# Optimization experiments

Hardware: AMD Instinct MI355X
Metric: run time of the kernel (lower is better)

Reference implementation:

```python
import jax, jax.numpy as jnp
import numpy as np

D = 1024      # d_model
E = 8         # initial_experts
H = 4 * D     # expert FFN hidden
CAP_F = 1.25  # capacity_factor
VOCAB = 256


def setup_inputs() -> dict:
    key = jax.random.key(0)
    ks = jax.random.split(key, 10)
    w = lambda k, shape, s: jax.random.normal(k, shape, jnp.float32) * s
    return dict(
        byte_seq=jax.random.randint(ks[0], (4, 2048), 0, VOCAB, jnp.int32),
        emb=w(ks[1], (VOCAB, D), 0.02),
        Wp=w(ks[2], (D, D), 1.0 / np.sqrt(D)), bp=jnp.zeros((D,), jnp.float32),
        Wg=w(ks[3], (D, D), 1.0 / np.sqrt(D)), bg=jnp.zeros((D,), jnp.float32),
        Wr=w(ks[4], (D, E), 1.0 / np.sqrt(D)), br=jnp.zeros((E,), jnp.float32),
        W1=w(ks[5], (E, D, H), 1.0 / np.sqrt(D)), b1=jnp.zeros((E, H), jnp.float32),
        W2=w(ks[6], (E, H, D), 1.0 / np.sqrt(H)), b2=jnp.zeros((E, D), jnp.float32),
        Wh=w(ks[7], (D, VOCAB), 1.0 / np.sqrt(D)), bh=jnp.zeros((VOCAB,), jnp.float32),
    )


def reference(byte_seq, emb, Wp, bp, Wg, bg, Wr, br, W1, b1, W2, b2, Wh, bh):
    # ---- byte embedding ----
    x = emb[byte_seq]                                 # [B,T,D]
    B, T, _ = x.shape

    # ---- SSM core: precompute input projections, scan only the recurrence ----
    px = x @ Wp + bp                                   # [B,T,D]
    gx = jax.nn.sigmoid(x @ Wg + bg)                   # [B,T,D]

    def step(state, inp):
        p, g = inp
        state = jnp.tanh(p + state)
        return state, g * state

    s0 = jnp.zeros((B, D), x.dtype)
    next_state, ys = jax.lax.scan(step, s0, (px.transpose(1, 0, 2), gx.transpose(1, 0, 2)))
    y = ys.transpose(1, 0, 2)                          # [B,T,D]

    # ---- capacity-limited top-1 MoE routing ----
    xf = y.reshape(-1, D)                              # [N,D]
    N = xf.shape[0]
    probs = jax.nn.softmax(xf @ Wr + br, axis=-1)      # [N,E]
    top = jnp.argmax(probs, axis=-1)                   # [N]
    onehot = jax.nn.one_hot(top, E, dtype=xf.dtype)    # [N,E]
    pos = jnp.cumsum(onehot, axis=0) * onehot          # 1-based slot within expert
    capacity = int(CAP_F * N / E)
    keep = (pos > 0) & (pos <= capacity)               # [N,E] tokens within capacity
    gate = jnp.take_along_axis(probs, top[:, None], axis=-1)[:, 0]  # [N]
    scale = gate * keep.any(axis=-1).astype(xf.dtype)

    # grouped expert FFN (fixed small loop over experts, masked combine)
    out = jnp.zeros_like(xf)
    for e in range(E):
        h = jax.nn.gelu(xf @ W1[e] + b1[e])            # [N,H]
        oe = h @ W2[e] + b2[e]                         # [N,D]
        out = out + oe * keep[:, e].astype(xf.dtype)[:, None]
    out = out * scale[:, None]

    entropy_loss = -jnp.mean(jnp.sum(probs * jnp.log(probs + 1e-9), axis=-1))
    expert_counts = jnp.sum(onehot, axis=0)

    logits = out.reshape(B, T, D) @ Wh + bh            # [B,T,256]
    return logits, next_state, entropy_loss, expert_counts
```

## Files before the change

### kernel.cpp

```cpp
#include <hip/hip_runtime.h>
#include <hip/hip_bf16.h>
#include <cstdint>
#include <cstddef>

#define AS1 __attribute__((address_space(1)))
#define AS3 __attribute__((address_space(3)))

typedef __hip_bfloat16 bf16;
typedef float f32x4 __attribute__((ext_vector_type(4)));
typedef short bf16x8 __attribute__((ext_vector_type(8)));

#define B_     4
#define T_     2048
#define D_     1024
#define E_     8
#define H_     4096
#define NTOK   8192
#define CAP    1280
#define VOCAB_ 256

static constexpr size_t OFF_PG    = 0;
static constexpr size_t OFF_Y     = 2097152;
static constexpr size_t OFF_TOP   = 35651584;
static constexpr size_t OFF_GATE  = 35684352;
static constexpr size_t OFF_ENT   = 35717120;
static constexpr size_t OFF_CNT   = 35749888;
static constexpr size_t OFF_CKEPT = 35750144;
static constexpr size_t OFF_SLOT  = 35750400;
static constexpr size_t OFF_XE    = 35791360;
static constexpr size_t OFF_HE    = 56762880;
static constexpr size_t OFF_WT    = 140648960;
static constexpr size_t OFF_WHT   = 207757824;
static constexpr size_t OFF_OUTB  = 208282112;

#define LOGITS_OFF 0
#define NS_OFF     2097152
#define ENT_OFF    2101248
#define CNT_OFF    2101249

__device__ __forceinline__ void gll16(const void* g, void* l) {
  __builtin_amdgcn_global_load_lds((AS1 const void*)g, (AS3 void*)l, 16, 0, 0);
}
__device__ __forceinline__ unsigned short f2bu(float f) {
  bf16 h = __float2bfloat16(f);
  return __builtin_bit_cast(unsigned short, h);
}
__device__ __forceinline__ float bu2f(unsigned short u) {
  unsigned int x = ((unsigned int)u) << 16;
  return __builtin_bit_cast(float, x);
}
__device__ __forceinline__ float fast_tanh(float z) {
  float e2 = __expf(z + z);
  return fmaf(-2.f, __builtin_amdgcn_rcpf(e2 + 1.f), 1.f);
}

__global__ __launch_bounds__(256) void slv_embproj_part(
    const float* __restrict__ emb, const float* __restrict__ Wp,
    const float* __restrict__ Wg,
    float* __restrict__ Ppart, float* __restrict__ Gpart) {
  __shared__ float embT[128][9];
  int rb = blockIdx.x, kc = blockIdx.y;
  int r0 = rb * 8, k0 = kc * 128;
  int tid = threadIdx.x;
  int c = tid * 4;
  {
    int i4 = tid * 4;
    int r = i4 >> 7, kb = i4 & 127;
    f32x4 v = *reinterpret_cast<const f32x4*>(emb + (size_t)(r0 + r) * D_ + k0 + kb);
    embT[kb + 0][r] = v.x; embT[kb + 1][r] = v.y;
    embT[kb + 2][r] = v.z; embT[kb + 3][r] = v.w;
  }
  __syncthreads();
  f32x4 aP[8] = {}, aG[8] = {};
  #pragma unroll 4
  for (int kk = 0; kk < 128; ++kk) {
    f32x4 wp = *reinterpret_cast<const f32x4*>(Wp + (size_t)(k0 + kk) * D_ + c);
    f32x4 wg = *reinterpret_cast<const f32x4*>(Wg + (size_t)(k0 + kk) * D_ + c);
    #pragma unroll
    for (int r = 0; r < 8; ++r) {
      float e = embT[kk][r];
      aP[r] += e * wp;
      aG[r] += e * wg;
    }
  }
  #pragma unroll
  for (int r = 0; r < 8; ++r) {
    size_t o = ((size_t)kc * 256 + r0 + r) * D_ + c;
    *reinterpret_cast<f32x4*>(Ppart + o) = aP[r];
    *reinterpret_cast<f32x4*>(Gpart + o) = aG[r];
  }
}

__global__ __launch_bounds__(256) void slv_embproj_reduce(
    const float* __restrict__ Ppart, const float* __restrict__ Gpart,
    const float* __restrict__ bp, const float* __restrict__ bg,
    float2* __restrict__ PG) {
  int i = blockIdx.x * 256 + threadIdx.x;
  int r = i >> 8;
  int c = (i & 255) * 4;
  f32x4 sp = {}, sg = {};
  #pragma unroll
  for (int kc = 0; kc < 8; ++kc) {
    size_t o = ((size_t)kc * 256 + r) * D_ + c;
    sp += *reinterpret_cast<const f32x4*>(Ppart + o);
    sg += *reinterpret_cast<const f32x4*>(Gpart + o);
  }
  sp += *reinterpret_cast<const f32x4*>(bp + c);
  sg += *reinterpret_cast<const f32x4*>(bg + c);
  f32x4 g;
  g.x = 1.f / (1.f + __expf(-sg.x));
  g.y = 1.f / (1.f + __expf(-sg.y));
  g.z = 1.f / (1.f + __expf(-sg.z));
  g.w = 1.f / (1.f + __expf(-sg.w));
  f32x4 st0 = { sp.x, g.x, sp.y, g.y };
  f32x4 st1 = { sp.z, g.z, sp.w, g.w };
  f32x4* dst = reinterpret_cast<f32x4*>(PG + (size_t)r * D_ + c);
  dst[0] = st0; dst[1] = st1;
}

__global__ __launch_bounds__(256) void slv_gatherpg(
    const int* __restrict__ bytes, const float2* __restrict__ PG,
    float2* __restrict__ pg_seq) {
  int t0 = blockIdx.x * 16;
  __shared__ int bl[16];
  if (threadIdx.x < 16) bl[threadIdx.x] = bytes[t0 + threadIdx.x];
  __syncthreads();
  int c = threadIdx.x * 4;
  #pragma unroll 4
  for (int u = 0; u < 16; ++u) {
    const f32x4* src = (const f32x4*)(PG + (size_t)bl[u] * D_ + c);
    f32x4* dst = (f32x4*)(pg_seq + (size_t)(t0 + u) * D_ + c);
    f32x4 v0 = src[0], v1 = src[1];
    dst[0] = v0; dst[1] = v1;
  }
}

#define SU 16
__global__ __launch_bounds__(64, 1) void slv_scan(
    const float2* __restrict__ pg_seq,
    float* __restrict__ y, float* __restrict__ ns) {
  int b = blockIdx.x >> 4;
  int d = (blockIdx.x & 15) * 64 + threadIdx.x;
  const float2* pp = pg_seq + (size_t)b * T_ * D_ + d;
  float* yp = y + (size_t)b * T_ * D_ + d;
  float2 pA[SU], pB[SU];
  #pragma unroll
  for (int u = 0; u < SU; ++u) pA[u] = pp[(size_t)u * D_];
  float s = 0.f;
  for (int t0 = 0; t0 < T_; t0 += 2 * SU) {
    #pragma unroll
    for (int u = 0; u < SU; ++u) pB[u] = pp[(size_t)(t0 + SU + u) * D_];
    #pragma unroll
    for (int u = 0; u < SU; ++u) {
      s = fast_tanh(pA[u].x + s);
      yp[(size_t)(t0 + u) * D_] = pA[u].y * s;
    }
    if (t0 + 2 * SU < T_) {
      #pragma unroll
      for (int u = 0; u < SU; ++u) pA[u] = pp[(size_t)(t0 + 2 * SU + u) * D_];
    }
    #pragma unroll
    for (int u = 0; u < SU; ++u) {
      s = fast_tanh(pB[u].x + s);
      yp[(size_t)(t0 + SU + u) * D_] = pB[u].y * s;
    }
  }
  ns[b * D_ + d] = s;
}

__global__ __launch_bounds__(256) void slv_router(
    const float* __restrict__ y, const float* __restrict__ Wr, const float* __restrict__ br,
    int* __restrict__ top, float* __restrict__ gate, float* __restrict__ entTok,
    int* __restrict__ countsInt) {
  int wave = threadIdx.x >> 6, lane = threadIdx.x & 63;
  int tok = blockIdx.x * 4 + wave;
  const float* yr = y + (size_t)tok * D_;
  float acc[E_];
  #pragma unroll
  for (int e = 0; e < E_; ++e) acc[e] = 0.f;
  for (int i = 0; i < 16; ++i) {
    int d = i * 64 + lane;
    float v = yr[d];
    const float4* w = (const float4*)(Wr + d * E_);
    float4 w0 = w[0], w1 = w[1];
    acc[0] = fmaf(v, w0.x, acc[0]); acc[1] = fmaf(v, w0.y, acc[1]);
    acc[2] = fmaf(v, w0.z, acc[2]); acc[3] = fmaf(v, w0.w, acc[3]);
    acc[4] = fmaf(v, w1.x, acc[4]); acc[5] = fmaf(v, w1.y, acc[5]);
    acc[6] = fmaf(v, w1.z, acc[6]); acc[7] = fmaf(v, w1.w, acc[7]);
  }
  #pragma unroll
  for (int off = 32; off; off >>= 1)
    #pragma unroll
    for (int e = 0; e < E_; ++e) acc[e] += __shfl_xor(acc[e], off);
  if (lane == 0) {
    float l[E_], p[E_];
    float mx = -1e30f;
    #pragma unroll
    for (int e = 0; e < E_; ++e) { l[e] = acc[e] + br[e]; mx = fmaxf(mx, l[e]); }
    float sum = 0.f;
    #pragma unroll
    for (int e = 0; e < E_; ++e) { p[e] = expf(l[e] - mx); sum += p[e]; }
    float inv = 1.f / sum;
    int bestE = 0; float bestP = -1.f; float ent = 0.f;
    #pragma unroll
    for (int e = 0; e < E_; ++e) {
      float pe = p[e] * inv;
      ent += pe * logf(pe + 1e-9f);
      if (pe > bestP) { bestP = pe; bestE = e; }
    }
    top[tok] = bestE; gate[tok] = bestP; entTok[tok] = ent;
    atomicAdd(&countsInt[bestE], 1);
  }
}

__global__ __launch_bounds__(256) void slv_capacity(
    const int* __restrict__ top, int* __restrict__ slotTok, int* __restrict__ cntKept) {
  __shared__ unsigned char tops[NTOK];
  __shared__ int sb[256];
  int tid = threadIdx.x;
  for (int i = tid; i < NTOK; i += 256) tops[i] = (unsigned char)top[i];
  __syncthreads();
  int cnt[E_];
  #pragma unroll
  for (int e = 0; e < E_; ++e) cnt[e] = 0;
  int n0 = tid * 32;
  for (int i = 0; i < 32; ++i) {
    int v = tops[n0 + i];
    #pragma unroll
    for (int e = 0; e < E_; ++e) cnt[e] += (v == e) ? 1 : 0;
  }
  int base[E_];
  for (int e = 0; e < E_; ++e) {
    sb[tid] = cnt[e];
    __syncthreads();
    for (int off = 1; off < 256; off <<= 1) {
      int add = (tid >= off) ? sb[tid - off] : 0;
      __syncthreads();
      sb[tid] += add;
      __syncthreads();
    }
    base[e] = sb[tid] - cnt[e];
    if (tid == 0) cntKept[e] = min(sb[255], CAP);
    __syncthreads();
  }
  for (int i = 0; i < 32; ++i) {
    int n = n0 + i;
    int v = tops[n];
    #pragma unroll
    for (int e = 0; e < E_; ++e) {
      if (v == e) {
        int r = base[e]++;
        if (r < CAP) slotTok[e * CAP + r] = n;
      }
    }
  }
}

__global__ __launch_bounds__(256) void slv_gather(
    const float* __restrict__ y, const int* __restrict__ slotTok,
    const int* __restrict__ cntKept, unsigned short* __restrict__ Xe) {
  int slot = blockIdx.x;
  int e = slot / CAP, r = slot % CAP;
  int c4 = threadIdx.x * 4;
  ushort4 o;
  if (r < cntKept[e]) {
    int tok = slotTok[slot];
    float4 v = *(const float4*)(y + (size_t)tok * D_ + c4);
    o.x = f2bu(v.x); o.y = f2bu(v.y); o.z = f2bu(v.z); o.w = f2bu(v.w);
  } else {
    o.x = 0; o.y = 0; o.z = 0; o.w = 0;
  }
  *(ushort4*)(Xe + (size_t)slot * D_ + c4) = o;
}

__global__ __launch_bounds__(256) void slv_transpose(
    const float* __restrict__ in, bf16* __restrict__ out, int R, int C) {
  __shared__ float tile[64][65];
  size_t mat = (size_t)blockIdx.z * R * C;
  int c0 = blockIdx.x * 64, r0 = blockIdx.y * 64;
  int tid = threadIdx.x;
  #pragma unroll
  for (int j = 0; j < 16; ++j) {
    int idx = j * 256 + tid; int r = idx >> 6, c = idx & 63;
    tile[r][c] = in[mat + (size_t)(r0 + r) * C + c0 + c];
  }
  __syncthreads();
  #pragma unroll
  for (int j = 0; j < 4; ++j) {
    int lin = j * 256 + tid;
    int cc = lin >> 4;
    int rr = (lin & 15) * 4;
    ushort4 v;
    v.x = f2bu(tile[rr + 0][cc]); v.y = f2bu(tile[rr + 1][cc]);
    v.z = f2bu(tile[rr + 2][cc]); v.w = f2bu(tile[rr + 3][cc]);
    *(ushort4*)((unsigned short*)out + mat + (size_t)(c0 + cc) * R + r0 + rr) = v;
  }
}

__device__ __forceinline__ void gemm_core(
    const char* ga, const char* gb, int K, bf16* As, bf16* Bs,
    f32x4 (&acc)[4][4], int wave, int lane, int wr, int wc) {
  const int Krow = K * 2;
  for (int ks = 0; ks < K; ks += 64) {
    #pragma unroll
    for (int rnd = 0; rnd < 4; ++rnd) {
      int chunk = rnd * 4 + wave;
      int o = chunk * 1024 + lane * 16;
      int row = o >> 7, col = o & 127;
      int scol = col ^ ((row & 7) << 4);
      size_t gofs = (size_t)row * Krow + (size_t)ks * 2 + scol;
      gll16(ga + gofs, (char*)As + chunk * 1024);
      gll16(gb + gofs, (char*)Bs + chunk * 1024);
    }
    __syncthreads();
    #pragma unroll
    for (int kk = 0; kk < 2; ++kk) {
      bf16x8 a[4], b[4];
      int koff = kk * 64 + ((lane >> 4) << 4);
      #pragma unroll
      for (int m = 0; m < 4; ++m) {
        int row = wr * 64 + m * 16 + (lane & 15);
        int sc = koff ^ ((row & 7) << 4);
        a[m] = *(const bf16x8*)((const char*)As + row * 128 + sc);
      }
      #pragma unroll
      for (int n = 0; n < 4; ++n) {
        int row = wc * 64 + n * 16 + (lane & 15);
        int sc = koff ^ ((row & 7) << 4);
        b[n] = *(const bf16x8*)((const char*)Bs + row * 128 + sc);
      }
      #pragma unroll
      for (int m = 0; m < 4; ++m)
        #pragma unroll
        for (int n = 0; n < 4; ++n)
          acc[m][n] = __builtin_amdgcn_mfma_f32_16x16x32_bf16(a[m], b[n], acc[m][n], 0, 0, 0);
    }
    __syncthreads();
  }
}

__device__ __forceinline__ void gemm256_core(
    const char* ga, const char* gb, size_t krow, size_t kbyte0, int NT,
    char* lds, int tid, int lane, int wr, int wc, f32x4 (&acc)[8][4]) {
  auto STAGE = [&](int kt) {
    char* lb = lds + (kt & 1) * 65536;
    #pragma unroll
    for (int h = 0; h < 4; ++h) {
      const char* g = (h < 2) ? ga : gb;
      #pragma unroll
      for (int c2 = 0; c2 < 2; ++c2) {
        int o = c2 * 8192 + tid * 16;
        int row = o >> 7, col = o & 127;
        int scol = col ^ ((row & 7) << 4);
        size_t gofs = (size_t)((h & 1) * 128 + row) * krow + kbyte0 + (size_t)kt * 128 + scol;
        gll16(g + gofs, lb + h * 16384 + o);
      }
    }
  };
  int koff16 = (lane >> 4) << 4;
  STAGE(0);
  for (int kt = 0; kt < NT; ++kt) {
    __builtin_amdgcn_s_barrier();
    if (kt + 1 < NT) {
      STAGE(kt + 1);
      asm volatile("s_waitcnt vmcnt(8)" ::: "memory");
    } else {
      asm volatile("s_waitcnt vmcnt(0)" ::: "memory");
    }
    __builtin_amdgcn_s_barrier();
    __builtin_amdgcn_sched_barrier(0);
    const char* Ab = lds + (kt & 1) * 65536;
    const char* Bb = Ab + 32768;
    bf16x8 b0[4], b1[4];
    #pragma unroll
    for (int n = 0; n < 4; ++n) {
      int row = wc * 64 + n * 16 + (lane & 15);
      const char* base = Bb + row * 128;
      int sw = (row & 7) << 4;
      b0[n] = *(const bf16x8*)(base + (koff16 ^ sw));
      b1[n] = *(const bf16x8*)(base + ((64 + koff16) ^ sw));
    }
    #pragma unroll
    for (int mp = 0; mp < 4; ++mp) {
      bf16x8 a0[2], a1[2];
      #pragma unroll
      for (int i = 0; i < 2; ++i) {
        int row = wr * 128 + (mp * 2 + i) * 16 + (lane & 15);
        const char* base = Ab + row * 128;
        int sw = (row & 7) << 4;
        a0[i] = *(const bf16x8*)(base + (koff16 ^ sw));
        a1[i] = *(const bf16x8*)(base + ((64 + koff16) ^ sw));
      }
      __builtin_amdgcn_s_setprio(1);
      #pragma unroll
      for (int i = 0; i < 2; ++i) {
        int m = mp * 2 + i;
        #pragma unroll
        for (int n = 0; n < 4; ++n)
          acc[m][n] = __builtin_amdgcn_mfma_f32_16x16x32_bf16(a0[i], b0[n], acc[m][n], 0, 0, 0);
        #pragma unroll
        for (int n = 0; n < 4; ++n)
          acc[m][n] = __builtin_amdgcn_mfma_f32_16x16x32_bf16(a1[i], b1[n], acc[m][n], 0, 0, 0);
      }
      __builtin_amdgcn_s_setprio(0);
    }
  }
}

__global__ __launch_bounds__(512, 2) void slv_ffn1_g(
    const bf16* __restrict__ Xe, const bf16* __restrict__ W1t, const float* __restrict__ b1,
    const int* __restrict__ cntKept, unsigned short* __restrict__ He) {
  int e = blockIdx.z, mt = blockIdx.y, nt = blockIdx.x;
  if (mt * 256 >= cntKept[e]) return;
  extern __shared__ char lds[];
  int tid = threadIdx.x, wave = tid >> 6, lane = tid & 63;
  int wr = wave >> 2, wc = wave & 3;
  const char* ga = (const char*)(Xe + ((size_t)e * CAP + mt * 256) * D_);
  const char* gb = (const char*)(W1t + ((size_t)e * H_ + nt * 256) * D_);
  f32x4 acc[8][4] = {};
  gemm256_core(ga, gb, (size_t)D_ * 2, 0, D_ / 64, lds, tid, lane, wr, wc, acc);
  size_t slot0 = (size_t)e * CAP + mt * 256;
  int colb = nt * 256 + wc * 64;
  #pragma unroll
  for (int m = 0; m < 8; ++m) {
    int trow0 = wr * 128 + m * 16 + ((lane >> 4) << 2);
    #pragma unroll
    for (int n = 0; n < 4; ++n) {
      int col = colb + n * 16 + (lane & 15);
      float bias = b1[e * H_ + col];
      #pragma unroll
      for (int r = 0; r < 4; ++r) {
        float x = acc[m][n][r] + bias;
        float t = fast_tanh(0.7978845608028654f * (x + 0.044715f * x * x * x));
        float gel = 0.5f * x * (1.f + t);
        He[(slot0 + trow0 + r) * (size_t)H_ + col] = f2bu(gel);
      }
    }
  }
}

__global__ __launch_bounds__(512, 2) void slv_ffn2_part(
    const bf16* __restrict__ He, const bf16* __restrict__ W2t,
    const int* __restrict__ cntKept,
    unsigned short* __restrict__ part0, unsigned short* __restrict__ part1) {
  int ez = blockIdx.z;
  int e = ez >> 1, s = ez & 1;
  int mt = blockIdx.y, nt = blockIdx.x;
  if (mt * 256 >= cntKept[e]) return;
  extern __shared__ char lds[];
  int tid = threadIdx.x, wave = tid >> 6, lane = tid & 63;
  int wr = wave >> 2, wc = wave & 3;
  const char* ga = (const char*)(He + ((size_t)e * CAP + mt * 256) * H_);
  const char* gb = (const char*)(W2t + ((size_t)e * D_ + nt * 256) * H_);
  f32x4 acc[8][4] = {};
  gemm256_core(ga, gb, (size_t)H_ * 2, (size_t)s * 2048 * 2, 2048 / 64,
               lds, tid, lane, wr, wc, acc);
  unsigned short* part = s ? part1 : part0;
  size_t slot0 = (size_t)e * CAP + mt * 256;
  int colb = nt * 256 + wc * 64;
  #pragma unroll
  for (int m = 0; m < 8; ++m) {
    int trow0 = wr * 128 + m * 16 + ((lane >> 4) << 2);
    #pragma unroll
    for (int n = 0; n < 4; ++n) {
      int col = colb + n * 16 + (lane & 15);
      #pragma unroll
      for (int r = 0; r < 4; ++r)
        part[(slot0 + trow0 + r) * (size_t)D_ + col] = f2bu(acc[m][n][r]);
    }
  }
}

__global__ __launch_bounds__(256) void slv_ffn2_reduce(
    const unsigned short* __restrict__ part0, const unsigned short* __restrict__ part1,
    const float* __restrict__ b2, const int* __restrict__ cntKept,
    const int* __restrict__ slotTok, const float* __restrict__ gate,
    unsigned short* __restrict__ outb) {
  int slot = blockIdx.x;
  int e = slot / CAP, r = slot % CAP;
  if (r >= cntKept[e]) return;
  int tok = slotTok[slot];
  float sc = gate[tok];
  int c4 = threadIdx.x * 4;
  ushort4 p0 = *(const ushort4*)(part0 + (size_t)slot * D_ + c4);
  ushort4 p1 = *(const ushort4*)(part1 + (size_t)slot * D_ + c4);
  const float4 bb = *(const float4*)(b2 + e * D_ + c4);
  ushort4 o;
  o.x = f2bu((bu2f(p0.x) + bu2f(p1.x) + bb.x) * sc);
  o.y = f2bu((bu2f(p0.y) + bu2f(p1.y) + bb.y) * sc);
  o.z = f2bu((bu2f(p0.z) + bu2f(p1.z) + bb.z) * sc);
  o.w = f2bu((bu2f(p0.w) + bu2f(p1.w) + bb.w) * sc);
  *(ushort4*)(outb + (size_t)tok * D_ + c4) = o;
}

__global__ __launch_bounds__(256) void slv_head(
    const bf16* __restrict__ outb, const bf16* __restrict__ Wht, const float* __restrict__ bh,
    float* __restrict__ logits) {
  int nt = blockIdx.x, mt = blockIdx.y;
  __shared__ __align__(16) bf16 As[128 * 64], Bs[128 * 64];
  int tid = threadIdx.x, wave = tid >> 6, lane = tid & 63;
  int wr = wave >> 1, wc = wave & 1;
  const char* ga = (const char*)(outb + (size_t)mt * 128 * D_);
  const char* gb = (const char*)(Wht + (size_t)nt * 128 * D_);
  f32x4 acc[4][4] = {};
  gemm_core(ga, gb, D_, As, Bs, acc, wave, lane, wr, wc);
  int colb = nt * 128 + wc * 64;
  #pragma unroll
  for (int m = 0; m < 4; ++m) {
    int trow0 = wr * 64 + m * 16 + ((lane >> 4) << 2);
    #pragma unroll
    for (int n = 0; n < 4; ++n) {
      int col = colb + n * 16 + (lane & 15);
      float bias = bh[col];
      #pragma unroll
      for (int r = 0; r < 4; ++r) {
        int row = mt * 128 + trow0 + r;
        logits[(size_t)row * VOCAB_ + col] = acc[m][n][r] + bias;
      }
    }
  }
}

__global__ __launch_bounds__(256) void slv_finalize(
    const float* __restrict__ entTok, const int* __restrict__ countsInt,
    float* __restrict__ out) {
  __shared__ float red[256];
  int tid = threadIdx.x;
  float s = 0.f;
  for (int i = tid; i < NTOK; i += 256) s += entTok[i];
  red[tid] = s;
  __syncthreads();
  for (int off = 128; off; off >>= 1) {
    if (tid < off) red[tid] += red[tid + off];
    __syncthreads();
  }
  if (tid == 0) out[ENT_OFF] = -red[0] / (float)NTOK;
  if (tid < E_) out[CNT_OFF + tid] = (float)countsInt[tid];
}

extern "C" void kernel_launch(void* const* d_in, const int* in_sizes, int n_in,
                              void* d_out, int out_size, void* d_ws, size_t ws_size,
                              hipStream_t stream) {
  (void)in_sizes; (void)n_in; (void)out_size; (void)ws_size;
  const int*   byte_seq = (const int*)d_in[0];
  const float* emb = (const float*)d_in[1];
  const float* Wp  = (const float*)d_in[2];
  const float* bp  = (const float*)d_in[3];
  const float* Wg  = (const float*)d_in[4];
  const float* bg  = (const float*)d_in[5];
  const float* Wr  = (const float*)d_in[6];
  const float* br  = (const float*)d_in[7];
  const float* W1  = (const float*)d_in[8];
  const float* b1  = (const float*)d_in[9];
  const float* W2  = (const float*)d_in[10];
  const float* b2  = (const float*)d_in[11];
  const float* Wh  = (const float*)d_in[12];
  const float* bh  = (const float*)d_in[13];
  float* out = (float*)d_out;

  char* ws = (char*)d_ws;
  float2* PG      = (float2*)(ws + OFF_PG);
  float* y        = (float*)(ws + OFF_Y);
  int*   top      = (int*)(ws + OFF_TOP);
  float* gate     = (float*)(ws + OFF_GATE);
  float* entTok   = (float*)(ws + OFF_ENT);
  int*   countsInt= (int*)(ws + OFF_CNT);
  int*   cntKept  = (int*)(ws + OFF_CKEPT);
  int*   slotTok  = (int*)(ws + OFF_SLOT);
  unsigned short* Xe  = (unsigned short*)(ws + OFF_XE);
  unsigned short* He  = (unsigned short*)(ws + OFF_HE);
  bf16*  Wt       = (bf16*)(ws + OFF_WT);
  bf16*  Wht      = (bf16*)(ws + OFF_WHT);
  unsigned short* outb = (unsigned short*)(ws + OFF_OUTB);
  float*  Ppart   = (float*)(ws + OFF_HE);
  float*  Gpart   = (float*)(ws + OFF_HE + 8388608);
  float2* pg_seq  = (float2*)(ws + OFF_HE);
  unsigned short* part0 = (unsigned short*)(ws + OFF_Y);
  unsigned short* part1 = (unsigned short*)(ws + OFF_XE);

  hipFuncSetAttribute(reinterpret_cast<const void*>(slv_ffn1_g),
                      hipFuncAttributeMaxDynamicSharedMemorySize, 131072);
  hipFuncSetAttribute(reinterpret_cast<const void*>(slv_ffn2_part),
                      hipFuncAttributeMaxDynamicSharedMemorySize, 131072);

  hipMemsetAsync(countsInt, 0, E_ * sizeof(int), stream);
  hipMemsetAsync(outb, 0, (size_t)NTOK * D_ * 2, stream);

  slv_embproj_part<<<dim3(32, 8), 256, 0, stream>>>(emb, Wp, Wg, Ppart, Gpart);
  slv_embproj_reduce<<<256, 256, 0, stream>>>(Ppart, Gpart, bp, bg, PG);
  slv_gatherpg<<<NTOK / 16, 256, 0, stream>>>(byte_seq, PG, pg_seq);
  slv_scan<<<64, 64, 0, stream>>>(pg_seq, y, out + NS_OFF);
  slv_router<<<NTOK / 4, 256, 0, stream>>>(y, Wr, br, top, gate, entTok, countsInt);
  slv_capacity<<<1, 256, 0, stream>>>(top, slotTok, cntKept);
  slv_gather<<<E_ * CAP, 256, 0, stream>>>(y, slotTok, cntKept, Xe);

  slv_transpose<<<dim3(4, 16, 1), 256, 0, stream>>>(Wh, Wht, 1024, 256);
  slv_transpose<<<dim3(64, 16, 8), 256, 0, stream>>>(W1, Wt, 1024, 4096);
  slv_ffn1_g<<<dim3(16, 5, 8), 512, 131072, stream>>>((const bf16*)Xe, Wt, b1, cntKept, He);
  slv_transpose<<<dim3(16, 64, 8), 256, 0, stream>>>(W2, Wt, 4096, 1024);
  slv_ffn2_part<<<dim3(4, 5, 16), 512, 131072, stream>>>((const bf16*)He, Wt, cntKept, part0, part1);
  slv_ffn2_reduce<<<E_ * CAP, 256, 0, stream>>>(part0, part1, b2, cntKept, slotTok, gate, outb);
  slv_head<<<dim3(2, 64), 256, 0, stream>>>((const bf16*)outb, Wht, bh, out + LOGITS_OFF);
  slv_finalize<<<1, 256, 0, stream>>>(entTok, countsInt, out);
}
```

Before: 577.5 us.

## Rework expert GEMM core into 4-stage pipeline and use wave-shuffle capacity scan

The shared 256x256 GEMM core used by both expert FFN kernels moves from a double-buffered K=64 loop to a four-slot ring of K=32 stages. Loads are issued three stages ahead and split into two halves interleaved with two MFMA phases, with finer vmcnt waits and barriers, to hide global-load latency. The capacity kernel's 8 serial block-wide LDS prefix scans are replaced by packed 16-bit counters scanned with wavefront shuffles plus a small cross-wave fixup, removing many syncthreads. This adds more barriers per K step and a new LDS row/column remapping whose correctness relies on matching the fragment layout.

```diff
diff --git a/kernel.cpp b/kernel.cpp
--- a/kernel.cpp
+++ b/kernel.cpp
@@ -216,32 +216,49 @@
 __global__ __launch_bounds__(256) void slv_capacity(
     const int* __restrict__ top, int* __restrict__ slotTok, int* __restrict__ cntKept) {
   __shared__ unsigned char tops[NTOK];
-  __shared__ int sb[256];
-  int tid = threadIdx.x;
+  __shared__ unsigned int wt[4][4];
+  int tid = threadIdx.x, lane = tid & 63, w = tid >> 6;
   for (int i = tid; i < NTOK; i += 256) tops[i] = (unsigned char)top[i];
   __syncthreads();
-  int cnt[E_];
-  #pragma unroll
-  for (int e = 0; e < E_; ++e) cnt[e] = 0;
+  unsigned int c0 = 0, c1 = 0, c2 = 0, c3 = 0;
   int n0 = tid * 32;
   for (int i = 0; i < 32; ++i) {
     int v = tops[n0 + i];
-    #pragma unroll
-    for (int e = 0; e < E_; ++e) cnt[e] += (v == e) ? 1 : 0;
-  }
+    unsigned inc = 1u << ((v & 1) << 4);
+    int hi = v >> 1;
+    if (hi == 0) c0 += inc;
+    else if (hi == 1) c1 += inc;
+    else if (hi == 2) c2 += inc;
+    else c3 += inc;
+  }
+  unsigned int s0 = c0, s1 = c1, s2 = c2, s3 = c3;
+  #pragma unroll
+  for (int off = 1; off < 64; off <<= 1) {
+    unsigned int t0 = (unsigned)__shfl_up((int)s0, off);
+    unsigned int t1 = (unsigned)__shfl_up((int)s1, off);
+    unsigned int t2 = (unsigned)__shfl_up((int)s2, off);
+    unsigned int t3 = (unsigned)__shfl_up((int)s3, off);
+    if (lane >= off) { s0 += t0; s1 += t1; s2 += t2; s3 += t3; }
+  }
+  if (lane == 63) { wt[w][0] = s0; wt[w][1] = s1; wt[w][2] = s2; wt[w][3] = s3; }
+  __syncthreads();
+  unsigned int p0 = 0, p1 = 0, p2 = 0, p3 = 0;
+  for (int i = 0; i < w; ++i) { p0 += wt[i][0]; p1 += wt[i][1]; p2 += wt[i][2]; p3 += wt[i][3]; }
+  unsigned int e0 = s0 - c0 + p0, e1 = s1 - c1 + p1, e2 = s2 - c2 + p2, e3 = s3 - c3 + p3;
   int base[E_];
-  for (int e = 0; e < E_; ++e) {
-    sb[tid] = cnt[e];
-    __syncthreads();
-    for (int off = 1; off < 256; off <<= 1) {
-      int add = (tid >= off) ? sb[tid - off] : 0;
-      __syncthreads();
-      sb[tid] += add;
-      __syncthreads();
-    }
-    base[e] = sb[tid] - cnt[e];
-    if (tid == 0) cntKept[e] = min(sb[255], CAP);
-    __syncthreads();
+  base[0] = e0 & 0xffff; base[1] = e0 >> 16;
+  base[2] = e1 & 0xffff; base[3] = e1 >> 16;
+  base[4] = e2 & 0xffff; base[5] = e2 >> 16;
+  base[6] = e3 & 0xffff; base[7] = e3 >> 16;
+  if (tid == 0) {
+    unsigned int t0t = wt[0][0] + wt[1][0] + wt[2][0] + wt[3][0];
+    unsigned int t1t = wt[0][1] + wt[1][1] + wt[2][1] + wt[3][1];
+    unsigned int t2t = wt[0][2] + wt[1][2] + wt[2][2] + wt[3][2];
+    unsigned int t3t = wt[0][3] + wt[1][3] + wt[2][3] + wt[3][3];
+    cntKept[0] = min((int)(t0t & 0xffff), CAP); cntKept[1] = min((int)(t0t >> 16), CAP);
+    cntKept[2] = min((int)(t1t & 0xffff), CAP); cntKept[3] = min((int)(t1t >> 16), CAP);
+    cntKept[4] = min((int)(t2t & 0xffff), CAP); cntKept[5] = min((int)(t2t >> 16), CAP);
+    cntKept[6] = min((int)(t3t & 0xffff), CAP); cntKept[7] = min((int)(t3t >> 16), CAP);
   }
   for (int i = 0; i < 32; ++i) {
     int n = n0 + i;
@@ -339,71 +356,67 @@
   }
 }
 
-__device__ __forceinline__ void gemm256_core(
-    const char* ga, const char* gb, size_t krow, size_t kbyte0, int NT,
+__device__ __forceinline__ void gemm256_8p(
+    const char* ga, const char* gb, size_t krow, size_t kbyte0, int NH,
     char* lds, int tid, int lane, int wr, int wc, f32x4 (&acc)[8][4]) {
-  auto STAGE = [&](int kt) {
-    char* lb = lds + (kt & 1) * 65536;
-    #pragma unroll
-    for (int h = 0; h < 4; ++h) {
-      const char* g = (h < 2) ? ga : gb;
-      #pragma unroll
-      for (int c2 = 0; c2 < 2; ++c2) {
-        int o = c2 * 8192 + tid * 16;
-        int row = o >> 7, col = o & 127;
-        int scol = col ^ ((row & 7) << 4);
-        size_t gofs = (size_t)((h & 1) * 128 + row) * krow + kbyte0 + (size_t)kt * 128 + scol;
-        gll16(g + gofs, lb + h * 16384 + o);
-      }
-    }
+  auto STG = [&](int h, int r) {
+    int o = (r & 1) * 8192 + tid * 16;
+    int l = o >> 7, rem = o & 127;
+    int rem2 = rem ^ ((l & 7) << 4);
+    int row = 2 * l + (rem2 >> 6);
+    int kb = rem2 & 63;
+    const char* g = (r < 2) ? ga : gb;
+    size_t gofs = (size_t)row * krow + kbyte0 + (size_t)h * 64 + kb;
+    gll16(g + gofs, lds + (h & 3) * 32768 + ((r < 2) ? 0 : 16384) + o);
   };
-  int koff16 = (lane >> 4) << 4;
-  STAGE(0);
-  for (int kt = 0; kt < NT; ++kt) {
+  int l15 = lane & 15;
+  int lhalf = l15 >> 1;
+  int aoff = (((lane & 1) << 6) | ((lane >> 4) << 4)) ^ (lhalf << 4);
+  STG(0, 0); STG(0, 1); STG(0, 2); STG(0, 3);
+  STG(1, 0); STG(1, 1); STG(1, 2); STG(1, 3);
+  STG(2, 0); STG(2, 1); STG(2, 2); STG(2, 3);
+  asm volatile("s_waitcnt vmcnt(8)" ::: "memory");
+  __builtin_amdgcn_s_barrier();
+  for (int h = 0; h < NH; ++h) {
+    const char* Ab = lds + (h & 3) * 32768;
+    const char* Bb = Ab + 16384;
+    bf16x8 a[4], b[4];
+    #pragma unroll
+    for (int n = 0; n < 4; ++n)
+      b[n] = *(const bf16x8*)(Bb + 128 * (wc * 32 + n * 8 + lhalf) + aoff);
+    #pragma unroll
+    for (int m = 0; m < 4; ++m)
+      a[m] = *(const bf16x8*)(Ab + 128 * (wr * 64 + m * 8 + lhalf) + aoff);
+    if (h + 3 < NH) { STG(h + 3, 0); STG(h + 3, 1); }
     __builtin_amdgcn_s_barrier();
-    if (kt + 1 < NT) {
-      STAGE(kt + 1);
-      asm volatile("s_waitcnt vmcnt(8)" ::: "memory");
-    } else {
-      asm volatile("s_waitcnt vmcnt(0)" ::: "memory");
-    }
+    asm volatile("s_waitcnt lgkmcnt(0)" ::: "memory");
+    __builtin_amdgcn_sched_barrier(0);
+    __builtin_amdgcn_s_setprio(1);
+    #pragma unroll
+    for (int m = 0; m < 4; ++m)
+      #pragma unroll
+      for (int n = 0; n < 4; ++n)
+        acc[m][n] = __builtin_amdgcn_mfma_f32_16x16x32_bf16(a[m], b[n], acc[m][n], 0, 0, 0);
+    __builtin_amdgcn_s_setprio(0);
     __builtin_amdgcn_s_barrier();
+    #pragma unroll
+    for (int m = 0; m < 4; ++m)
+      a[m] = *(const bf16x8*)(Ab + 128 * (wr * 64 + (m + 4) * 8 + lhalf) + aoff);
+    if (h + 3 < NH) { STG(h + 3, 2); STG(h + 3, 3); }
+    if (h + 3 <= NH - 1)      asm volatile("s_waitcnt vmcnt(8)" ::: "memory");
+    else if (h + 2 == NH - 1) asm volatile("s_waitcnt vmcnt(4)" ::: "memory");
+    else if (h + 1 == NH - 1) asm volatile("s_waitcnt vmcnt(0)" ::: "memory");
+    __builtin_amdgcn_s_barrier();
+    asm volatile("s_waitcnt lgkmcnt(0)" ::: "memory");
     __builtin_amdgcn_sched_barrier(0);
-    const char* Ab = lds + (kt & 1) * 65536;
-    const char* Bb = Ab + 32768;
-    bf16x8 b0[4], b1[4];
-    #pragma unroll
-    for (int n = 0; n < 4; ++n) {
-      int row = wc * 64 + n * 16 + (lane & 15);
-      const char* base = Bb + row * 128;
-      int sw = (row & 7) << 4;
-      b0[n] = *(const bf16x8*)(base + (koff16 ^ sw));
-      b1[n] = *(const bf16x8*)(base + ((64 + koff16) ^ sw));
-    }
-    #pragma unroll
-    for (int mp = 0; mp < 4; ++mp) {
-      bf16x8 a0[2], a1[2];
-      #pragma unroll
-      for (int i = 0; i < 2; ++i) {
-        int row = wr * 128 + (mp * 2 + i) * 16 + (lane & 15);
-        const char* base = Ab + row * 128;
-        int sw = (row & 7) << 4;
-        a0[i] = *(const bf16x8*)(base + (koff16 ^ sw));
-        a1[i] = *(const bf16x8*)(base + ((64 + koff16) ^ sw));
-      }
-      __builtin_amdgcn_s_setprio(1);
-      #pragma unroll
-      for (int i = 0; i < 2; ++i) {
-        int m = mp * 2 + i;
-        #pragma unroll
-        for (int n = 0; n < 4; ++n)
-          acc[m][n] = __builtin_amdgcn_mfma_f32_16x16x32_bf16(a0[i], b0[n], acc[m][n], 0, 0, 0);
-        #pragma unroll
-        for (int n = 0; n < 4; ++n)
-          acc[m][n] = __builtin_amdgcn_mfma_f32_16x16x32_bf16(a1[i], b1[n], acc[m][n], 0, 0, 0);
-      }
-      __builtin_amdgcn_s_setprio(0);
-    }
+    __builtin_amdgcn_s_setprio(1);
+    #pragma unroll
+    for (int m = 0; m < 4; ++m)
+      #pragma unroll
+      for (int n = 0; n < 4; ++n)
+        acc[m + 4][n] = __builtin_amdgcn_mfma_f32_16x16x32_bf16(a[m], b[n], acc[m + 4][n], 0, 0, 0);
+    __builtin_amdgcn_s_setprio(0);
+    __builtin_amdgcn_s_barrier();
   }
 }
 
@@ -418,7 +431,7 @@
   const char* ga = (const char*)(Xe + ((size_t)e * CAP + mt * 256) * D_);
   const char* gb = (const char*)(W1t + ((size_t)e * H_ + nt * 256) * D_);
   f32x4 acc[8][4] = {};
-  gemm256_core(ga, gb, (size_t)D_ * 2, 0, D_ / 64, lds, tid, lane, wr, wc, acc);
+  gemm256_8p(ga, gb, (size_t)D_ * 2, 0, D_ / 32, lds, tid, lane, wr, wc, acc);
   size_t slot0 = (size_t)e * CAP + mt * 256;
   int colb = nt * 256 + wc * 64;
   #pragma unroll
@@ -453,8 +466,8 @@
   const char* ga = (const char*)(He + ((size_t)e * CAP + mt * 256) * H_);
   const char* gb = (const char*)(W2t + ((size_t)e * D_ + nt * 256) * H_);
   f32x4 acc[8][4] = {};
-  gemm256_core(ga, gb, (size_t)H_ * 2, (size_t)s * 2048 * 2, 2048 / 64,
-               lds, tid, lane, wr, wc, acc);
+  gemm256_8p(ga, gb, (size_t)H_ * 2, (size_t)s * 2048 * 2, 2048 / 32,
+             lds, tid, lane, wr, wc, acc);
   unsigned short* part = s ? part1 : part0;
   size_t slot0 = (size_t)e * CAP + mt * 256;
   int colb = nt * 256 + wc * 64;
```

Measured after the change: 570.5 us. About the same (-1.2%).
